# Performance work log

Measured on AMD Instinct MI355X. Metric: run time of the kernel, lower is better.

The kernel has to match this reference:

```python
import jax, jax.numpy as jnp
import numpy as np

N_NODES = 100000
N_EDGES = 1600000
IN_FEATS, HIDDEN_FEATS, OUT_FEATS = 32, 64, 16


def setup_inputs() -> dict:
    key = jax.random.key(0)
    ks = jax.random.split(key, 8)
    return {
        "features": jax.random.normal(ks[0], (N_NODES, IN_FEATS), dtype=jnp.float32),
        "src": jax.random.randint(ks[1], (N_EDGES,), 0, N_NODES, dtype=jnp.int64),
        "dst": jax.random.randint(ks[2], (N_EDGES,), 0, N_NODES, dtype=jnp.int64),
        "W1_self": jax.random.normal(ks[3], (IN_FEATS, HIDDEN_FEATS), dtype=jnp.float32) * 0.1,
        "W1_neigh": jax.random.normal(ks[4], (IN_FEATS, HIDDEN_FEATS), dtype=jnp.float32) * 0.1,
        "b1": jnp.zeros((HIDDEN_FEATS,), dtype=jnp.float32),
        "W2_self": jax.random.normal(ks[5], (HIDDEN_FEATS, OUT_FEATS), dtype=jnp.float32) * 0.1,
        "W2_neigh": jax.random.normal(ks[6], (HIDDEN_FEATS, OUT_FEATS), dtype=jnp.float32) * 0.1,
        "b2": jnp.zeros((OUT_FEATS,), dtype=jnp.float32),
    }


def _sage_conv_mean(h, src, dst, n_nodes, W_self, W_neigh, b):
    # DGL SAGEConv(mean): gather src features to edges, mean-reduce at dst,
    # then fc_self(h) + fc_neigh(mean_neigh) + bias.
    ones = jnp.ones(src.shape, dtype=h.dtype)
    deg = jax.ops.segment_sum(ones, dst, num_segments=n_nodes)  # in-degree [N]
    agg = jax.ops.segment_sum(h[src], dst, num_segments=n_nodes)  # [N, d]
    mean_neigh = agg / jnp.maximum(deg, 1.0)[:, None]
    return h @ W_self + mean_neigh @ W_neigh + b


def reference(features, src, dst, W1_self, W1_neigh, b1, W2_self, W2_neigh, b2):
    n = features.shape[0]
    h = _sage_conv_mean(features, src, dst, n, W1_self, W1_neigh, b1)
    h = jax.nn.relu(h)
    # dropout is identity at inference (Keras call default training=False)
    out = _sage_conv_mean(h, src, dst, n, W2_self, W2_neigh, b2)
    return out
```

## Files before the change

### kernel.cpp

```cpp
#include <hip/hip_runtime.h>

#define N_NODES 100000
#define N_EDGES 1600000
#define IN_F 32
#define HID_F 64
#define OUT_F 16
#define BSIZE 512
#define NBKT 256
#define CAP 10240
#define CHUNK 4096
#define NBUCK ((N_NODES + BSIZE - 1) / BSIZE)
#define APITCH 68

__global__ __launch_bounds__(NBKT) void cursor_init_kernel(int* __restrict__ cursor) {
  cursor[threadIdx.x] = threadIdx.x * CAP;
}

__global__ __launch_bounds__(512) void bucket_kernel(
    const int* __restrict__ src, const int* __restrict__ dst,
    int* __restrict__ cursor, unsigned* __restrict__ sorted) {
  __shared__ unsigned stage[CHUNK];
  __shared__ unsigned char sbkt[CHUNK];
  __shared__ int lcnt[NBKT], lscan[NBKT], gbase[NBKT];
  int t = threadIdx.x;
  if (t < NBKT) lcnt[t] = 0;
  __syncthreads();

  int base = blockIdx.x * CHUNK;
  unsigned mypk[CHUNK / 512];
  int myb[CHUNK / 512], myrank[CHUNK / 512];
#pragma unroll
  for (int i = 0; i < CHUNK / 512; ++i) {
    int e = base + t + 512 * i;
    if (e < N_EDGES) {
      unsigned s = (unsigned)src[e], d = (unsigned)dst[e];
      myb[i] = (int)(d >> 9);
      mypk[i] = (s << 9) | (d & 511u);
      myrank[i] = atomicAdd(&lcnt[myb[i]], 1);
    } else {
      myb[i] = -1;
    }
  }
  __syncthreads();
  if (t < NBKT) lscan[t] = lcnt[t];
  __syncthreads();
  for (int off = 1; off < NBKT; off <<= 1) {
    int v = (t < NBKT && t >= off) ? lscan[t - off] : 0;
    __syncthreads();
    if (t < NBKT) lscan[t] += v;
    __syncthreads();
  }
  if (t < NBKT) gbase[t] = lcnt[t] ? atomicAdd(&cursor[t], lcnt[t]) : 0;
  __syncthreads();
#pragma unroll
  for (int i = 0; i < CHUNK / 512; ++i) {
    if (myb[i] >= 0) {
      int slot = (lscan[myb[i]] - lcnt[myb[i]]) + myrank[i];
      stage[slot] = mypk[i];
      sbkt[slot] = (unsigned char)myb[i];
    }
  }
  __syncthreads();
  int nvalid = min(CHUNK, N_EDGES - base);
  for (int i = t; i < nvalid; i += 512) {
    unsigned p = stage[i];
    int b = (int)sbkt[i];
    int addr = gbase[b] + (i - (lscan[b] - lcnt[b]));
    sorted[addr] = p;
  }
}

__global__ __launch_bounds__(1024) void bcsr_kernel(
    const unsigned* __restrict__ sorted, const int* __restrict__ cursor,
    int* __restrict__ ptr, int* __restrict__ col) {
  __shared__ int lcnt[BSIZE];
  __shared__ int lcur[BSIZE];
  __shared__ int scanbuf[BSIZE];
  int t = threadIdx.x;
  int b = blockIdx.x;
  int base = b * CAP;
  int ne = cursor[b] - base;

  if (t < BSIZE) lcnt[t] = 0;
  __syncthreads();
  for (int i = t; i < ne; i += 1024)
    atomicAdd(&lcnt[sorted[base + i] & (BSIZE - 1)], 1);
  __syncthreads();

  int c = 0;
  if (t < BSIZE) { c = lcnt[t]; scanbuf[t] = c; }
  __syncthreads();
  for (int off = 1; off < BSIZE; off <<= 1) {
    int u = (t < BSIZE && t >= off) ? scanbuf[t - off] : 0;
    __syncthreads();
    if (t < BSIZE) scanbuf[t] += u;
    __syncthreads();
  }
  if (t < BSIZE) {
    int incl = scanbuf[t];
    lcur[t] = base + incl - c;
    int v = b * BSIZE + t;
    if (v < N_NODES) ptr[v] = base + incl;
  }
  __syncthreads();

  for (int i = t; i < ne; i += 1024) {
    unsigned p = sorted[base + i];
    int pos = atomicAdd(&lcur[p & (BSIZE - 1)], 1);
    col[pos] = (int)(p >> 9);
  }
}

__global__ __launch_bounds__(256) void gather1_kernel(
    const int* __restrict__ ptr, const int* __restrict__ col,
    const float* __restrict__ feat, float* __restrict__ meanf) {
  int gid = blockIdx.x * 256 + threadIdx.x;
  int v = gid >> 3;
  int f4 = gid & 7;
  int start = (v & (BSIZE - 1)) ? ptr[v - 1] : (v >> 9) * CAP;
  int end = ptr[v];
  const float4* F = (const float4*)feat;
  float4 s0 = {0.f, 0.f, 0.f, 0.f}, s1 = {0.f, 0.f, 0.f, 0.f};
  float4 s2 = {0.f, 0.f, 0.f, 0.f}, s3 = {0.f, 0.f, 0.f, 0.f};
  int e = start;
  for (; e + 3 < end; e += 4) {
    int c0 = col[e], c1 = col[e + 1], c2 = col[e + 2], c3 = col[e + 3];
    float4 a = F[c0 * 8 + f4];
    float4 b = F[c1 * 8 + f4];
    float4 cc = F[c2 * 8 + f4];
    float4 d = F[c3 * 8 + f4];
    s0.x += a.x; s0.y += a.y; s0.z += a.z; s0.w += a.w;
    s1.x += b.x; s1.y += b.y; s1.z += b.z; s1.w += b.w;
    s2.x += cc.x; s2.y += cc.y; s2.z += cc.z; s2.w += cc.w;
    s3.x += d.x; s3.y += d.y; s3.z += d.z; s3.w += d.w;
  }
  for (; e < end; ++e) {
    float4 a = F[col[e] * 8 + f4];
    s0.x += a.x; s0.y += a.y; s0.z += a.z; s0.w += a.w;
  }
  float inv = 1.0f / fmaxf((float)(end - start), 1.0f);
  float4 r;
  r.x = (s0.x + s1.x + s2.x + s3.x) * inv;
  r.y = (s0.y + s1.y + s2.y + s3.y) * inv;
  r.z = (s0.z + s1.z + s2.z + s3.z) * inv;
  r.w = (s0.w + s1.w + s2.w + s3.w) * inv;
  ((float4*)meanf)[v * 8 + f4] = r;
}

__global__ __launch_bounds__(256) void l1t2s2_kernel(
    const float* __restrict__ feat, const float* __restrict__ meanf,
    const float* __restrict__ W1s, const float* __restrict__ W1n,
    const float* __restrict__ b1,
    const float* __restrict__ W2n, const float* __restrict__ W2s,
    float* __restrict__ t2, float* __restrict__ s2) {
  __shared__ float sA[64 * APITCH];
  __shared__ float sW[64 * 64];

  int t = threadIdx.x;
  int tile = blockIdx.x * 64;
  int nvalid = min(64, N_NODES - tile);

  {
    const float4* Fg = (const float4*)(feat + (size_t)tile * IN_F);
    const float4* Mg = (const float4*)(meanf + (size_t)tile * IN_F);
    int lim = nvalid * 8;
#pragma unroll
    for (int it = 0; it < 2; ++it) {
      int idx = t + 256 * it;
      int n = idx >> 3, c = idx & 7;
      if (idx < lim) {
        float4 a = Fg[idx];
        sA[(4 * c + 0) * APITCH + n] = a.x;
        sA[(4 * c + 1) * APITCH + n] = a.y;
        sA[(4 * c + 2) * APITCH + n] = a.z;
        sA[(4 * c + 3) * APITCH + n] = a.w;
        float4 m = Mg[idx];
        sA[(32 + 4 * c + 0) * APITCH + n] = m.x;
        sA[(32 + 4 * c + 1) * APITCH + n] = m.y;
        sA[(32 + 4 * c + 2) * APITCH + n] = m.z;
        sA[(32 + 4 * c + 3) * APITCH + n] = m.w;
      }
    }
  }
  {
    float4* Ws = (float4*)sW;
#pragma unroll
    for (int it = 0; it < 4; ++it) {
      int idx = t + 256 * it;
      int row = idx >> 4;
      const float4* srcw = (row < 32) ? (const float4*)W1s : (const float4*)W1n;
      Ws[idx] = srcw[(row & 31) * 16 + (idx & 15)];
    }
  }
  int tx = t & 15, ty = t >> 4;
  int n0 = 4 * ty, c0 = 4 * tx;
  float4 bb = ((const float4*)b1)[tx];
  __syncthreads();

  float acc[4][4];
#pragma unroll
  for (int i = 0; i < 4; ++i) { acc[i][0] = bb.x; acc[i][1] = bb.y; acc[i][2] = bb.z; acc[i][3] = bb.w; }
#pragma unroll 4
  for (int k = 0; k < 64; ++k) {
    float4 a = *(const float4*)&sA[k * APITCH + n0];
    float4 w = *(const float4*)&sW[k * 64 + c0];
    acc[0][0] += a.x * w.x; acc[0][1] += a.x * w.y; acc[0][2] += a.x * w.z; acc[0][3] += a.x * w.w;
    acc[1][0] += a.y * w.x; acc[1][1] += a.y * w.y; acc[1][2] += a.y * w.z; acc[1][3] += a.y * w.w;
    acc[2][0] += a.z * w.x; acc[2][1] += a.z * w.y; acc[2][2] += a.z * w.z; acc[2][3] += a.z * w.w;
    acc[3][0] += a.w * w.x; acc[3][1] += a.w * w.y; acc[3][2] += a.w * w.z; acc[3][3] += a.w * w.w;
  }
  __syncthreads();

#pragma unroll
  for (int jj = 0; jj < 4; ++jj) {
    float4 v;
    v.x = fmaxf(acc[0][jj], 0.0f);
    v.y = fmaxf(acc[1][jj], 0.0f);
    v.z = fmaxf(acc[2][jj], 0.0f);
    v.w = fmaxf(acc[3][jj], 0.0f);
    *(float4*)&sA[(c0 + jj) * APITCH + n0] = v;
  }
  {
    float4* Ws = (float4*)sW;
#pragma unroll
    for (int it = 0; it < 2; ++it) {
      int idx = t + 256 * it;
      int row = idx >> 3, ch = idx & 7;
      const float4* srcw = (ch < 4) ? (const float4*)W2n : (const float4*)W2s;
      Ws[row * 8 + ch] = srcw[row * 4 + (ch & 3)];
    }
  }
  __syncthreads();

  int c2 = 2 * tx;
  float a0 = 0.f, a1 = 0.f, b0 = 0.f, b1_ = 0.f, d0 = 0.f, d1 = 0.f, e0 = 0.f, e1 = 0.f;
#pragma unroll 4
  for (int k = 0; k < 64; ++k) {
    float4 a = *(const float4*)&sA[k * APITCH + n0];
    float2 w = *(const float2*)&sW[k * 32 + c2];
    a0 += a.x * w.x; a1 += a.x * w.y;
    b0 += a.y * w.x; b1_ += a.y * w.y;
    d0 += a.z * w.x; d1 += a.z * w.y;
    e0 += a.w * w.x; e1 += a.w * w.y;
  }
  {
    float rs[4][2] = {{a0, a1}, {b0, b1_}, {d0, d1}, {e0, e1}};
    float* outp = (c2 < 16) ? t2 : s2;
    int cc = c2 & 15;
#pragma unroll
    for (int i = 0; i < 4; ++i) {
      int v = tile + n0 + i;
      if (v < N_NODES) *(float2*)&outp[v * OUT_F + cc] = make_float2(rs[i][0], rs[i][1]);
    }
  }
}

__global__ __launch_bounds__(256) void gather2_final_kernel(
    const int* __restrict__ ptr, const int* __restrict__ col,
    const float* __restrict__ t2, const float* __restrict__ s2,
    const float* __restrict__ b2, float* __restrict__ out) {
  int gid = blockIdx.x * 256 + threadIdx.x;
  int v = gid >> 2;
  int c4 = gid & 3;
  if (v >= N_NODES) return;
  int start = (v & (BSIZE - 1)) ? ptr[v - 1] : (v >> 9) * CAP;
  int end = ptr[v];
  const float4* T = (const float4*)t2;
  float4 a0 = {0.f, 0.f, 0.f, 0.f}, a1 = {0.f, 0.f, 0.f, 0.f};
  float4 a2 = {0.f, 0.f, 0.f, 0.f}, a3 = {0.f, 0.f, 0.f, 0.f};
  int e = start;
  for (; e + 3 < end; e += 4) {
    int c0 = col[e], c1 = col[e + 1], c2 = col[e + 2], c3 = col[e + 3];
    float4 x = T[c0 * 4 + c4];
    float4 y = T[c1 * 4 + c4];
    float4 z = T[c2 * 4 + c4];
    float4 w = T[c3 * 4 + c4];
    a0.x += x.x; a0.y += x.y; a0.z += x.z; a0.w += x.w;
    a1.x += y.x; a1.y += y.y; a1.z += y.z; a1.w += y.w;
    a2.x += z.x; a2.y += z.y; a2.z += z.z; a2.w += z.w;
    a3.x += w.x; a3.y += w.y; a3.z += w.z; a3.w += w.w;
  }
  for (; e < end; ++e) {
    float4 x = T[col[e] * 4 + c4];
    a0.x += x.x; a0.y += x.y; a0.z += x.z; a0.w += x.w;
  }
  float inv = 1.0f / fmaxf((float)(end - start), 1.0f);
  float4 sv = ((const float4*)s2)[v * 4 + c4];
  float4 bv = ((const float4*)b2)[c4];
  float4 r;
  r.x = sv.x + bv.x + (a0.x + a1.x + a2.x + a3.x) * inv;
  r.y = sv.y + bv.y + (a0.y + a1.y + a2.y + a3.y) * inv;
  r.z = sv.z + bv.z + (a0.z + a1.z + a2.z + a3.z) * inv;
  r.w = sv.w + bv.w + (a0.w + a1.w + a2.w + a3.w) * inv;
  ((float4*)out)[v * 4 + c4] = r;
}

extern "C" void kernel_launch(void* const* d_in, const int* in_sizes, int n_in,
                              void* d_out, int out_size, void* d_ws, size_t ws_size,
                              hipStream_t stream) {
  const float* feat = (const float*)d_in[0];
  const int* src    = (const int*)d_in[1];
  const int* dst    = (const int*)d_in[2];
  const float* W1s  = (const float*)d_in[3];
  const float* W1n  = (const float*)d_in[4];
  const float* b1   = (const float*)d_in[5];
  const float* W2s  = (const float*)d_in[6];
  const float* W2n  = (const float*)d_in[7];
  const float* b2   = (const float*)d_in[8];
  float* out = (float*)d_out;

  const size_t N = N_NODES;
  const size_t SLAB = (size_t)NBKT * CAP;
  int* ptr = (int*)d_ws;
  int* col = ptr + N + 8;
  unsigned* sorted = (unsigned*)(col + SLAB);
  float* meanf = (float*)(sorted + SLAB);
  float* t2 = meanf + 32 * N;
  float* s2 = t2 + 16 * N;
  int* cursor = (int*)(s2 + 16 * N);

  cursor_init_kernel<<<1, NBKT, 0, stream>>>(cursor);
  bucket_kernel<<<(N_EDGES + CHUNK - 1) / CHUNK, 512, 0, stream>>>(src, dst, cursor, sorted);
  bcsr_kernel<<<NBUCK, 1024, 0, stream>>>(sorted, cursor, ptr, col);

  gather1_kernel<<<N_NODES * 8 / 256, 256, 0, stream>>>(ptr, col, feat, meanf);
  l1t2s2_kernel<<<(N_NODES + 63) / 64, 256, 0, stream>>>(feat, meanf, W1s, W1n, b1,
                                                         W2n, W2s, t2, s2);
  gather2_final_kernel<<<(N_NODES * 4 + 255) / 256, 256, 0, stream>>>(ptr, col, t2, s2,
                                                                      b2, out);
}
```

Before: 195.5 us.

## Gather neighbor features in bf16 to halve gather bandwidth

Adds a pre-pass that converts input features to bf16. Both gather kernels now read packed bf16 rows and accumulate in fp32, and the layer-1 kernel writes t2 as bf16. This halves the bytes moved by the random-access neighbor gathers, which dominate runtime. In exchange it adds a conversion kernel and loses precision in the aggregated features, which may exceed accuracy tolerances.

```diff
diff --git a/kernel.cpp b/kernel.cpp
--- a/kernel.cpp
+++ b/kernel.cpp
@@ -12,6 +12,34 @@
 #define NBUCK ((N_NODES + BSIZE - 1) / BSIZE)
 #define APITCH 68
 
+__device__ __forceinline__ unsigned f2bf(float f) {
+  unsigned u = __float_as_uint(f);
+  return (u + 0x7FFFu + ((u >> 16) & 1u)) >> 16;
+}
+
+#define ADD8(s, V) do { \
+  s[0] += __uint_as_float((V).x << 16); \
+  s[1] += __uint_as_float((V).x & 0xFFFF0000u); \
+  s[2] += __uint_as_float((V).y << 16); \
+  s[3] += __uint_as_float((V).y & 0xFFFF0000u); \
+  s[4] += __uint_as_float((V).z << 16); \
+  s[5] += __uint_as_float((V).z & 0xFFFF0000u); \
+  s[6] += __uint_as_float((V).w << 16); \
+  s[7] += __uint_as_float((V).w & 0xFFFF0000u); } while (0)
+
+__global__ __launch_bounds__(256) void f2bf_kernel(
+    const float4* __restrict__ in, uint4* __restrict__ outp) {
+  int i = blockIdx.x * 256 + threadIdx.x;
+  if (i >= N_NODES * IN_F / 8) return;
+  float4 a = in[2 * i], b = in[2 * i + 1];
+  uint4 r;
+  r.x = f2bf(a.x) | (f2bf(a.y) << 16);
+  r.y = f2bf(a.z) | (f2bf(a.w) << 16);
+  r.z = f2bf(b.x) | (f2bf(b.y) << 16);
+  r.w = f2bf(b.z) | (f2bf(b.w) << 16);
+  outp[i] = r;
+}
+
 __global__ __launch_bounds__(NBKT) void cursor_init_kernel(int* __restrict__ cursor) {
   cursor[threadIdx.x] = threadIdx.x * CAP;
 }
@@ -113,38 +141,34 @@
 
 __global__ __launch_bounds__(256) void gather1_kernel(
     const int* __restrict__ ptr, const int* __restrict__ col,
-    const float* __restrict__ feat, float* __restrict__ meanf) {
+    const uint4* __restrict__ featbf, float* __restrict__ meanf) {
   int gid = blockIdx.x * 256 + threadIdx.x;
-  int v = gid >> 3;
-  int f4 = gid & 7;
+  int v = gid >> 2;
+  int c = gid & 3;
+  if (v >= N_NODES) return;
   int start = (v & (BSIZE - 1)) ? ptr[v - 1] : (v >> 9) * CAP;
   int end = ptr[v];
-  const float4* F = (const float4*)feat;
-  float4 s0 = {0.f, 0.f, 0.f, 0.f}, s1 = {0.f, 0.f, 0.f, 0.f};
-  float4 s2 = {0.f, 0.f, 0.f, 0.f}, s3 = {0.f, 0.f, 0.f, 0.f};
+  float s[8] = {0.f, 0.f, 0.f, 0.f, 0.f, 0.f, 0.f, 0.f};
   int e = start;
   for (; e + 3 < end; e += 4) {
-    int c0 = col[e], c1 = col[e + 1], c2 = col[e + 2], c3 = col[e + 3];
-    float4 a = F[c0 * 8 + f4];
-    float4 b = F[c1 * 8 + f4];
-    float4 cc = F[c2 * 8 + f4];
-    float4 d = F[c3 * 8 + f4];
-    s0.x += a.x; s0.y += a.y; s0.z += a.z; s0.w += a.w;
-    s1.x += b.x; s1.y += b.y; s1.z += b.z; s1.w += b.w;
-    s2.x += cc.x; s2.y += cc.y; s2.z += cc.z; s2.w += cc.w;
-    s3.x += d.x; s3.y += d.y; s3.z += d.z; s3.w += d.w;
+    uint4 q0 = featbf[col[e] * 4 + c];
+    uint4 q1 = featbf[col[e + 1] * 4 + c];
+    uint4 q2 = featbf[col[e + 2] * 4 + c];
+    uint4 q3 = featbf[col[e + 3] * 4 + c];
+    ADD8(s, q0);
+    ADD8(s, q1);
+    ADD8(s, q2);
+    ADD8(s, q3);
   }
   for (; e < end; ++e) {
-    float4 a = F[col[e] * 8 + f4];
-    s0.x += a.x; s0.y += a.y; s0.z += a.z; s0.w += a.w;
+    uint4 q = featbf[col[e] * 4 + c];
+    ADD8(s, q);
   }
   float inv = 1.0f / fmaxf((float)(end - start), 1.0f);
-  float4 r;
-  r.x = (s0.x + s1.x + s2.x + s3.x) * inv;
-  r.y = (s0.y + s1.y + s2.y + s3.y) * inv;
-  r.z = (s0.z + s1.z + s2.z + s3.z) * inv;
-  r.w = (s0.w + s1.w + s2.w + s3.w) * inv;
-  ((float4*)meanf)[v * 8 + f4] = r;
+  float4 r0 = {s[0] * inv, s[1] * inv, s[2] * inv, s[3] * inv};
+  float4 r1 = {s[4] * inv, s[5] * inv, s[6] * inv, s[7] * inv};
+  ((float4*)meanf)[v * 8 + 2 * c] = r0;
+  ((float4*)meanf)[v * 8 + 2 * c + 1] = r1;
 }
 
 __global__ __launch_bounds__(256) void l1t2s2_kernel(
@@ -152,7 +176,7 @@
     const float* __restrict__ W1s, const float* __restrict__ W1n,
     const float* __restrict__ b1,
     const float* __restrict__ W2n, const float* __restrict__ W2s,
-    float* __restrict__ t2, float* __restrict__ s2) {
+    unsigned* __restrict__ t2u, float* __restrict__ s2) {
   __shared__ float sA[64 * APITCH];
   __shared__ float sW[64 * 64];
 
@@ -245,54 +269,63 @@
   }
   {
     float rs[4][2] = {{a0, a1}, {b0, b1_}, {d0, d1}, {e0, e1}};
-    float* outp = (c2 < 16) ? t2 : s2;
     int cc = c2 & 15;
 #pragma unroll
     for (int i = 0; i < 4; ++i) {
       int v = tile + n0 + i;
-      if (v < N_NODES) *(float2*)&outp[v * OUT_F + cc] = make_float2(rs[i][0], rs[i][1]);
+      if (v < N_NODES) {
+        if (c2 < 16) {
+          t2u[v * 8 + (cc >> 1)] = f2bf(rs[i][0]) | (f2bf(rs[i][1]) << 16);
+        } else {
+          *(float2*)&s2[v * OUT_F + cc] = make_float2(rs[i][0], rs[i][1]);
+        }
+      }
     }
   }
 }
 
 __global__ __launch_bounds__(256) void gather2_final_kernel(
     const int* __restrict__ ptr, const int* __restrict__ col,
-    const float* __restrict__ t2, const float* __restrict__ s2,
+    const uint4* __restrict__ t2bf, const float* __restrict__ s2,
     const float* __restrict__ b2, float* __restrict__ out) {
   int gid = blockIdx.x * 256 + threadIdx.x;
-  int v = gid >> 2;
-  int c4 = gid & 3;
+  int v = gid >> 1;
+  int c = gid & 1;
   if (v >= N_NODES) return;
   int start = (v & (BSIZE - 1)) ? ptr[v - 1] : (v >> 9) * CAP;
   int end = ptr[v];
-  const float4* T = (const float4*)t2;
-  float4 a0 = {0.f, 0.f, 0.f, 0.f}, a1 = {0.f, 0.f, 0.f, 0.f};
-  float4 a2 = {0.f, 0.f, 0.f, 0.f}, a3 = {0.f, 0.f, 0.f, 0.f};
+  float s[8] = {0.f, 0.f, 0.f, 0.f, 0.f, 0.f, 0.f, 0.f};
   int e = start;
   for (; e + 3 < end; e += 4) {
-    int c0 = col[e], c1 = col[e + 1], c2 = col[e + 2], c3 = col[e + 3];
-    float4 x = T[c0 * 4 + c4];
-    float4 y = T[c1 * 4 + c4];
-    float4 z = T[c2 * 4 + c4];
-    float4 w = T[c3 * 4 + c4];
-    a0.x += x.x; a0.y += x.y; a0.z += x.z; a0.w += x.w;
-    a1.x += y.x; a1.y += y.y; a1.z += y.z; a1.w += y.w;
-    a2.x += z.x; a2.y += z.y; a2.z += z.z; a2.w += z.w;
-    a3.x += w.x; a3.y += w.y; a3.z += w.z; a3.w += w.w;
+    uint4 q0 = t2bf[col[e] * 2 + c];
+    uint4 q1 = t2bf[col[e + 1] * 2 + c];
+    uint4 q2 = t2bf[col[e + 2] * 2 + c];
+    uint4 q3 = t2bf[col[e + 3] * 2 + c];
+    ADD8(s, q0);
+    ADD8(s, q1);
+    ADD8(s, q2);
+    ADD8(s, q3);
   }
   for (; e < end; ++e) {
-    float4 x = T[col[e] * 4 + c4];
-    a0.x += x.x; a0.y += x.y; a0.z += x.z; a0.w += x.w;
+    uint4 q = t2bf[col[e] * 2 + c];
+    ADD8(s, q);
   }
   float inv = 1.0f / fmaxf((float)(end - start), 1.0f);
-  float4 sv = ((const float4*)s2)[v * 4 + c4];
-  float4 bv = ((const float4*)b2)[c4];
-  float4 r;
-  r.x = sv.x + bv.x + (a0.x + a1.x + a2.x + a3.x) * inv;
-  r.y = sv.y + bv.y + (a0.y + a1.y + a2.y + a3.y) * inv;
-  r.z = sv.z + bv.z + (a0.z + a1.z + a2.z + a3.z) * inv;
-  r.w = sv.w + bv.w + (a0.w + a1.w + a2.w + a3.w) * inv;
-  ((float4*)out)[v * 4 + c4] = r;
+  float4 sv0 = ((const float4*)s2)[v * 4 + 2 * c];
+  float4 sv1 = ((const float4*)s2)[v * 4 + 2 * c + 1];
+  float4 bv0 = ((const float4*)b2)[2 * c];
+  float4 bv1 = ((const float4*)b2)[2 * c + 1];
+  float4 r0, r1;
+  r0.x = sv0.x + bv0.x + s[0] * inv;
+  r0.y = sv0.y + bv0.y + s[1] * inv;
+  r0.z = sv0.z + bv0.z + s[2] * inv;
+  r0.w = sv0.w + bv0.w + s[3] * inv;
+  r1.x = sv1.x + bv1.x + s[4] * inv;
+  r1.y = sv1.y + bv1.y + s[5] * inv;
+  r1.z = sv1.z + bv1.z + s[6] * inv;
+  r1.w = sv1.w + bv1.w + s[7] * inv;
+  ((float4*)out)[v * 4 + 2 * c] = r0;
+  ((float4*)out)[v * 4 + 2 * c + 1] = r1;
 }
 
 extern "C" void kernel_launch(void* const* d_in, const int* in_sizes, int n_in,
@@ -315,17 +348,21 @@
   int* col = ptr + N + 8;
   unsigned* sorted = (unsigned*)(col + SLAB);
   float* meanf = (float*)(sorted + SLAB);
-  float* t2 = meanf + 32 * N;
-  float* s2 = t2 + 16 * N;
-  int* cursor = (int*)(s2 + 16 * N);
-
+  float* s2 = meanf + 32 * N;
+  unsigned* featbf = (unsigned*)(s2 + 16 * N);
+  unsigned* t2u = featbf + 16 * N;
+  int* cursor = (int*)(t2u + 8 * N);
+
+  f2bf_kernel<<<(N_NODES * IN_F / 8 + 255) / 256, 256, 0, stream>>>(
+      (const float4*)feat, (uint4*)featbf);
   cursor_init_kernel<<<1, NBKT, 0, stream>>>(cursor);
   bucket_kernel<<<(N_EDGES + CHUNK - 1) / CHUNK, 512, 0, stream>>>(src, dst, cursor, sorted);
   bcsr_kernel<<<NBUCK, 1024, 0, stream>>>(sorted, cursor, ptr, col);
 
-  gather1_kernel<<<N_NODES * 8 / 256, 256, 0, stream>>>(ptr, col, feat, meanf);
+  gather1_kernel<<<(N_NODES * 4 + 255) / 256, 256, 0, stream>>>(
+      ptr, col, (const uint4*)featbf, meanf);
   l1t2s2_kernel<<<(N_NODES + 63) / 64, 256, 0, stream>>>(feat, meanf, W1s, W1n, b1,
-                                                         W2n, W2s, t2, s2);
-  gather2_final_kernel<<<(N_NODES * 4 + 255) / 256, 256, 0, stream>>>(ptr, col, t2, s2,
-                                                                      b2, out);
-}
+                                                         W2n, W2s, t2u, s2);
+  gather2_final_kernel<<<(N_NODES * 2 + 255) / 256, 256, 0, stream>>>(
+      ptr, col, (const uint4*)t2u, s2, b2, out);
+}
```

After: 190.4 us. 1.03x faster.
